# Kernel optimization log

Measured on AMD Instinct MI355X. Metric: run time of the kernel, lower is better.

Reference implementation:

```python
import jax, jax.numpy as jnp
import numpy as np

N = 50000        # num_nodes
E = 800000       # num_edges (avg degree 16)
K = 3            # Chebyshev order
F_IN = 144       # 144 * in_channels
F_OUT = 144      # 144 * out_channels


def setup_inputs() -> dict:
    key = jax.random.key(0)
    k1, k2, k3, k4, k5 = jax.random.split(key, 5)
    x = jax.random.normal(k1, (N, F_IN), dtype=jnp.float32)
    edge_index = jax.random.randint(k2, (2, E), 0, N, dtype=jnp.int32)
    edge_weight = jax.random.uniform(k3, (E,), dtype=jnp.float32)
    weight = jax.random.normal(k4, (K, F_IN, F_OUT), dtype=jnp.float32) * 0.02
    bias = jax.random.normal(k5, (F_OUT,), dtype=jnp.float32) * 0.02
    return {"x": x, "edge_index": edge_index, "edge_weight": edge_weight,
            "weight": weight, "bias": bias}


def reference(x, edge_index, edge_weight, weight, bias):
    row, col = edge_index[0], edge_index[1]
    # remove_self_loops: mask out edges with row == col (fixed-shape equivalent)
    mask = (row != col).astype(x.dtype)
    w = edge_weight * mask
    # degree over remaining edges, deg^-0.5 with inf -> 0
    deg = jax.ops.segment_sum(mask, row, num_segments=N)
    dinv = jnp.where(deg > 0, deg ** -0.5, jnp.zeros_like(deg))
    lap = -dinv[row] * w * dinv[col]  # [E]

    def spmm(v):  # out[i] = sum_{e: row_e = i} lap_e * v[col_e]
        return jax.ops.segment_sum(lap[:, None] * v[col], row, num_segments=N)

    Tx0 = x
    out = Tx0 @ weight[0]
    Tx1 = spmm(Tx0)
    out = out + Tx1 @ weight[1]
    for k in range(2, weight.shape[0]):
        Tx2 = 2.0 * spmm(Tx1) - Tx0
        out = out + Tx2 @ weight[k]
        Tx0, Tx1 = Tx1, Tx2
    return out + bias
```

## Files before the change

### kernel.cpp

```cpp
#include <hip/hip_runtime.h>
#include <hip/hip_bf16.h>

#define NN 50000
#define EE 800000
#define FF 144
#define NBLK 196
#define CVTBLK 1758
#define HISTBLK 3125

typedef __hip_bfloat16 bf16;
typedef __attribute__((ext_vector_type(8))) short short8;
typedef __attribute__((ext_vector_type(4))) float floatx4;
typedef __attribute__((ext_vector_type(2))) float float2v;

__device__ inline float blo(unsigned x) { return __uint_as_float(x << 16); }
__device__ inline float bhi(unsigned x) { return __uint_as_float(x & 0xffff0000u); }

__device__ inline void dec4fma(float* a, float l, unsigned d) {
    float2v p0 = __builtin_amdgcn_cvt_pk_f32_fp8((int)d, false);
    float2v p1 = __builtin_amdgcn_cvt_pk_f32_fp8((int)d, true);
    a[0] = fmaf(l, p0.x, a[0]);
    a[1] = fmaf(l, p0.y, a[1]);
    a[2] = fmaf(l, p1.x, a[2]);
    a[3] = fmaf(l, p1.y, a[3]);
}
__device__ inline void fma16q(float* a, float l, uint4 u) {
    dec4fma(a + 0, l, u.x);
    dec4fma(a + 4, l, u.y);
    dec4fma(a + 8, l, u.z);
    dec4fma(a + 12, l, u.w);
}
__device__ inline unsigned enc4(float a, float b, float c, float d) {
    int w = __builtin_amdgcn_cvt_pk_fp8_f32(a, b, 0, false);
    w = __builtin_amdgcn_cvt_pk_fp8_f32(c, d, w, true);
    return (unsigned)w;
}


__global__ void detect_k(const int* __restrict__ ei, int* __restrict__ flag) {
    __shared__ int nz;
    if (threadIdx.x == 0) nz = 0;
    __syncthreads();
    if (ei[2 * threadIdx.x + 1] != 0) atomicAdd(&nz, 1);
    __syncthreads();
    if (threadIdx.x == 0) *flag = (nz == 0) ? 1 : 0;
}

__device__ inline void load_edge(const int* ei, int e, int flag, int& r, int& c) {
    if (flag) { r = ei[2 * e]; c = ei[2 * EE + 2 * e]; }
    else      { r = ei[e];     c = ei[EE + e]; }
}


__global__ void cvthist_k(const float* __restrict__ x, bf16* __restrict__ xb,
                          unsigned char* __restrict__ xq,
                          const int* __restrict__ ei, int* __restrict__ cnt,
                          unsigned char* __restrict__ rank,
                          const int* __restrict__ flagp) {
    int b = blockIdx.x;
    if (b < CVTBLK) {
        int t = b * 256 + threadIdx.x;
        if (t >= NN * FF / 16) return;
        const float4* xp = (const float4*)x + t * 4;
        float4 v0 = xp[0], v1 = xp[1], v2 = xp[2], v3 = xp[3];
        float f[16] = {v0.x, v0.y, v0.z, v0.w, v1.x, v1.y, v1.z, v1.w,
                       v2.x, v2.y, v2.z, v2.w, v3.x, v3.y, v3.z, v3.w};
        unsigned short hs[16];
        #pragma unroll
        for (int j = 0; j < 16; ++j) {
            bf16 bb = (bf16)f[j];
            hs[j] = *(unsigned short*)&bb;
        }
        uint4* xbq = (uint4*)xb + t * 2;
        xbq[0] = ((uint4*)hs)[0];
        xbq[1] = ((uint4*)hs)[1];
        uint4 q;
        q.x = enc4(f[0], f[1], f[2], f[3]);
        q.y = enc4(f[4], f[5], f[6], f[7]);
        q.z = enc4(f[8], f[9], f[10], f[11]);
        q.w = enc4(f[12], f[13], f[14], f[15]);
        ((uint4*)xq)[t] = q;
    } else {
        int flag = *flagp;
        int e = (b - CVTBLK) * 256 + threadIdx.x;
        if (e >= EE) return;
        int r, c; load_edge(ei, e, flag, r, c);
        if (r != c) rank[e] = (unsigned char)atomicAdd(&cnt[r], 1);
    }
}


__global__ void cvtw_k(const float* __restrict__ wt, short* __restrict__ wtb) {
    int t = blockIdx.x * 256 + threadIdx.x;
    if (t >= 3 * FF * 168) return;
    int ph = t / (FF * 168);
    int rem = t - ph * FF * 168;
    int o = rem / 168;
    int i = rem - o * 168;
    short v = 0;
    if (i < FF) {
        bf16 b = (bf16)wt[ph * FF * FF + i * FF + o];
        v = *(const short*)&b;
    }
    wtb[t] = v;
}


__global__ void scan1_k(const int* __restrict__ cnt, int* __restrict__ rowptr,
                        int* __restrict__ bsum, float* __restrict__ dinv) {
    __shared__ int wsum[4], woff[4];
    int b = blockIdx.x, tid = threadIdx.x;
    int wv = tid >> 6, ln = tid & 63;
    int i = b * 256 + tid;
    int v = (i < NN) ? cnt[i] : 0;
    if (i < NN) dinv[i] = v > 0 ? rsqrtf((float)v) : 0.f;
    int x = v;
    #pragma unroll
    for (int off = 1; off < 64; off <<= 1) {
        int t = __shfl_up(x, off, 64);
        if (ln >= off) x += t;
    }
    if (ln == 63) wsum[wv] = x;
    __syncthreads();
    if (tid == 0) {
        int s = 0;
        #pragma unroll
        for (int j = 0; j < 4; ++j) { woff[j] = s; s += wsum[j]; }
        bsum[b] = s;
    }
    __syncthreads();
    if (i < NN) rowptr[i] = woff[wv] + (x - v);
}

__global__ void scan2_k(int* __restrict__ bsum, int* __restrict__ rowptr) {
    __shared__ int wsum[4], woff[4];
    int tid = threadIdx.x;
    int wv = tid >> 6, ln = tid & 63;
    int v = (tid < NBLK) ? bsum[tid] : 0;
    int x = v;
    #pragma unroll
    for (int off = 1; off < 64; off <<= 1) {
        int t = __shfl_up(x, off, 64);
        if (ln >= off) x += t;
    }
    if (ln == 63) wsum[wv] = x;
    __syncthreads();
    if (tid == 0) {
        int s = 0;
        #pragma unroll
        for (int j = 0; j < 4; ++j) { woff[j] = s; s += wsum[j]; }
        rowptr[NN] = s;
    }
    __syncthreads();
    if (tid < NBLK) bsum[tid] = woff[wv] + (x - v);
}

__global__ void scan3_k(int* __restrict__ rowptr, const int* __restrict__ bsum) {
    int b = blockIdx.x;
    int i = b * 256 + threadIdx.x;
    if (i < NN) rowptr[i] += bsum[b];
}


__global__ void scatter_k(const int* __restrict__ ei, const float* __restrict__ w,
                          const float* __restrict__ dinv, const int* __restrict__ rowptr,
                          const unsigned char* __restrict__ rank,
                          unsigned* __restrict__ pairs, const int* __restrict__ flagp) {
    int flag = *flagp;
    int e = blockIdx.x * 256 + threadIdx.x;
    if (e >= EE) return;
    int r, c; load_edge(ei, e, flag, r, c);
    if (r == c) return;
    int pos = rowptr[r] + (int)rank[e];
    float lap = -dinv[r] * dinv[c] * w[e];
    bf16 lb = (bf16)lap;
    pairs[pos] = (unsigned)c | ((unsigned)*(unsigned short*)&lb << 16);
}


template <int MODE>
__global__ void spmm_k(const unsigned char* __restrict__ vq, const bf16* __restrict__ x0,
                       const int* __restrict__ rowptr, const unsigned* __restrict__ pairs,
                       bf16* __restrict__ y, unsigned char* __restrict__ yq) {
    int t = blockIdx.x * 256 + threadIdx.x;
    if (t >= NN * 9) return;
    int i = t / 9;
    int fo = (t - i * 9) * 16;
    const unsigned char* vp = vq + fo;

    float a[16];
    #pragma unroll
    for (int j = 0; j < 16; ++j) a[j] = 0.f;

    int s = rowptr[i], e = rowptr[i + 1];
    int p = s;
    for (; p + 1 < e; p += 2) {
        unsigned pr0 = pairs[p], pr1 = pairs[p + 1];
        uint4 u0 = *(const uint4*)(vp + (pr0 & 0xffffu) * FF);
        uint4 u1 = *(const uint4*)(vp + (pr1 & 0xffffu) * FF);
        fma16q(a, bhi(pr0), u0);
        fma16q(a, bhi(pr1), u1);
    }
    if (p < e) {
        unsigned pr = pairs[p];
        uint4 u = *(const uint4*)(vp + (pr & 0xffffu) * FF);
        fma16q(a, bhi(pr), u);
    }

    if (MODE == 1) {
        const uint4* xp = (const uint4*)((const unsigned short*)x0 + i * FF + fo);
        uint4 u0 = xp[0], u1 = xp[1];
        a[0]  = 2.f * a[0]  - blo(u0.x);  a[1]  = 2.f * a[1]  - bhi(u0.x);
        a[2]  = 2.f * a[2]  - blo(u0.y);  a[3]  = 2.f * a[3]  - bhi(u0.y);
        a[4]  = 2.f * a[4]  - blo(u0.z);  a[5]  = 2.f * a[5]  - bhi(u0.z);
        a[6]  = 2.f * a[6]  - blo(u0.w);  a[7]  = 2.f * a[7]  - bhi(u0.w);
        a[8]  = 2.f * a[8]  - blo(u1.x);  a[9]  = 2.f * a[9]  - bhi(u1.x);
        a[10] = 2.f * a[10] - blo(u1.y);  a[11] = 2.f * a[11] - bhi(u1.y);
        a[12] = 2.f * a[12] - blo(u1.z);  a[13] = 2.f * a[13] - bhi(u1.z);
        a[14] = 2.f * a[14] - blo(u1.w);  a[15] = 2.f * a[15] - bhi(u1.w);
    }

    unsigned short hs[16];
    #pragma unroll
    for (int j = 0; j < 16; ++j) {
        bf16 b = (bf16)a[j];
        hs[j] = *(unsigned short*)&b;
    }
    uint4* yp = (uint4*)((unsigned short*)y + i * FF + fo);
    yp[0] = ((uint4*)hs)[0];
    yp[1] = ((uint4*)hs)[1];

    if (MODE == 0) {
        uint4 q;
        q.x = enc4(a[0], a[1], a[2], a[3]);
        q.y = enc4(a[4], a[5], a[6], a[7]);
        q.z = enc4(a[8], a[9], a[10], a[11]);
        q.w = enc4(a[12], a[13], a[14], a[15]);
        *(uint4*)(yq + i * FF + fo) = q;
    }
}


__global__ __launch_bounds__(1024)
void gemm_fused(const bf16* __restrict__ A0, const bf16* __restrict__ A1,
                const bf16* __restrict__ A2, const short* __restrict__ wtb,
                const float* __restrict__ bias, float* __restrict__ out) {
    __shared__ __align__(16) short Wt[3 * 144 * 168];
    int tid = threadIdx.x;

    {
        const uint4* Wg = (const uint4*)wtb;
        uint4* Wl = (uint4*)Wt;
        #pragma unroll
        for (int q = 0; q < 9; ++q) {
            int idx = q * 1024 + tid;
            if (idx < 9072) Wl[idx] = Wg[idx];
        }
    }
    __syncthreads();

    int wv = tid >> 6, ln = tid & 63;
    int m16 = ln & 15, quad = ln >> 4;
    int tile = wv * 256 + blockIdx.x;
    if (tile * 16 >= NN) return;
    int rowBase = tile * 16;
    int row = rowBase + m16;

    const bf16* const srcs[3] = {A0, A1, A2};
    const short8 zero8 = {0, 0, 0, 0, 0, 0, 0, 0};

    floatx4 acc[9];
    #pragma unroll
    for (int q = 0; q < 9; ++q) acc[q] = (floatx4){0.f, 0.f, 0.f, 0.f};

    #pragma unroll
    for (int ph = 0; ph < 3; ++ph) {
        const bf16* A = srcs[ph];
        short8 a[5];
        #pragma unroll
        for (int kt = 0; kt < 5; ++kt) {
            int k0 = kt * 32 + quad * 8;
            if (k0 < FF)
                a[kt] = *(const short8*)((const short*)A + row * FF + k0);
            else
                a[kt] = zero8;
        }

        const short* Wp = Wt + ph * 144 * 168;
        #pragma unroll
        for (int nt = 0; nt < 9; ++nt) {
            #pragma unroll
            for (int kt = 0; kt < 5; ++kt) {
                short8 b = *(const short8*)&Wp[(nt * 16 + m16) * 168 + kt * 32 + quad * 8];
                acc[nt] = __builtin_amdgcn_mfma_f32_16x16x32_bf16(a[kt], b, acc[nt], 0, 0, 0);
            }
        }
    }

    int rowc = rowBase + quad * 4;
    #pragma unroll
    for (int nt = 0; nt < 9; ++nt) {
        int col = nt * 16 + m16;
        float bs = bias[col];
        #pragma unroll
        for (int r = 0; r < 4; ++r) {
            int rr = rowc + r;
            out[rr * FF + col] = acc[nt][r] + bs;
        }
    }
}


extern "C" void kernel_launch(void* const* d_in, const int* in_sizes, int n_in,
                              void* d_out, int out_size, void* d_ws, size_t ws_size,
                              hipStream_t stream) {
    int ix = -1, iei = -1, iew = -1, iwt = -1, ib = -1;
    for (int i = 0; i < n_in; ++i) {
        switch (in_sizes[i]) {
            case NN * FF:      if (ix  < 0) ix  = i; break;
            case 2 * EE:       if (iei < 0) iei = i; break;
            case EE:           if (iew < 0) iew = i; break;
            case 3 * FF * FF:  if (iwt < 0) iwt = i; break;
            case FF:           if (ib  < 0) ib  = i; break;
        }
    }
    if (ix < 0 || iei < 0 || iew < 0 || iwt < 0 || ib < 0) {
        ix = 0; iei = 1; iew = 2; iwt = 3; ib = 4;
    }
    const float* x    = (const float*)d_in[ix];
    const int*   ei   = (const int*)d_in[iei];
    const float* ew   = (const float*)d_in[iew];
    const float* wt   = (const float*)d_in[iwt];
    const float* bias = (const float*)d_in[ib];
    float* out = (float*)d_out;

    char* p = (char*)d_ws;
    int*      cnt    = (int*)(p + 0);
    int*      rowptr = (int*)(p + 400000);
    float*    dinv   = (float*)(p + 600016);
    unsigned* pairs  = (unsigned*)(p + 800016);
    unsigned char* rank = (unsigned char*)(p + 4000016);
    bf16*     tx1    = (bf16*)(p + 7200016);
    bf16*     tx2    = (bf16*)(p + 21600016);
    short*    wtb    = (short*)(p + 36000016);
    int*      bsum   = (int*)(p + 36200000);
    unsigned char* xq   = (unsigned char*)(p + 36300000);
    unsigned char* tx1q = (unsigned char*)(p + 43600000);
    bf16*     xb     = (bf16*)(p + 64800016);
    int*      eflag  = (int*)(p + 79200016);

    if (ws_size < 79200032) return;

    hipMemsetAsync(d_ws, 0, 200000, stream);

    int spGrid   = (NN * 9 + 255) / 256;
    int wGrid    = (3 * FF * 168 + 255) / 256;

    detect_k<<<1, 256, 0, stream>>>(ei, eflag);
    cvthist_k<<<CVTBLK + HISTBLK, 256, 0, stream>>>(x, xb, xq, ei, cnt, rank, eflag);
    cvtw_k<<<wGrid, 256, 0, stream>>>(wt, wtb);
    scan1_k<<<NBLK, 256, 0, stream>>>(cnt, rowptr, bsum, dinv);
    scan2_k<<<1, 256, 0, stream>>>(bsum, rowptr);
    scan3_k<<<NBLK, 256, 0, stream>>>(rowptr, bsum);
    scatter_k<<<(EE + 255) / 256, 256, 0, stream>>>(ei, ew, dinv, rowptr, rank, pairs, eflag);

    spmm_k<0><<<spGrid, 256, 0, stream>>>(xq, xb, rowptr, pairs, tx1, tx1q);
    spmm_k<1><<<spGrid, 256, 0, stream>>>(tx1q, xb, rowptr, pairs, tx2, (unsigned char*)0);
    gemm_fused<<<256, 1024, 0, stream>>>(xb, tx1, tx2, wtb, bias, out);
}
```

Baseline: 218.5 us.

## Replace atomic-rank CSR build with two-level bucket sort of edges

Builds the CSR structure with a two-pass bucket sort instead of per-row global atomics. Edges are packed into 64-bit items and histogrammed per chunk into 128-row buckets in shared memory. After a prefix scan they are scattered into coarse buckets, then each bucket is finely sorted with shared-memory atomics to produce rowptr, dinv and the packed pairs. The weight conversion is also fused into the first kernel, the memset is removed, and one scan launch is dropped. In exchange the edge data takes extra passes through 64-bit intermediate buffers, and the order of edges within a row becomes nondeterministic.

```diff
diff --git a/kernel.cpp b/kernel.cpp
--- a/kernel.cpp
+++ b/kernel.cpp
@@ -4,9 +4,14 @@
 #define NN 50000
 #define EE 800000
 #define FF 144
-#define NBLK 196
 #define CVTBLK 1758
-#define HISTBLK 3125
+#define ECHK 2048
+#define NBE 391
+#define NBKT_REAL 391
+#define NBUCKET 392
+#define WGRID 284
+#define HM (NBUCKET * NBE)
+#define SCANBLK 599
 
 typedef __hip_bfloat16 bf16;
 typedef __attribute__((ext_vector_type(8))) short short8;
@@ -52,14 +57,17 @@
 }
 
 
-__global__ void cvthist_k(const float* __restrict__ x, bf16* __restrict__ xb,
-                          unsigned char* __restrict__ xq,
-                          const int* __restrict__ ei, int* __restrict__ cnt,
-                          unsigned char* __restrict__ rank,
-                          const int* __restrict__ flagp) {
+__global__ void fusedA_k(const float* __restrict__ x, bf16* __restrict__ xb,
+                         unsigned char* __restrict__ xq,
+                         const int* __restrict__ ei, const float* __restrict__ ew,
+                         unsigned long long* __restrict__ items, int* __restrict__ hist,
+                         const float* __restrict__ wt, short* __restrict__ wtb,
+                         const int* __restrict__ flagp) {
+    __shared__ int lh[NBUCKET];
     int b = blockIdx.x;
+    int tid = threadIdx.x;
     if (b < CVTBLK) {
-        int t = b * 256 + threadIdx.x;
+        int t = b * 256 + tid;
         if (t >= NN * FF / 16) return;
         const float4* xp = (const float4*)x + t * 4;
         float4 v0 = xp[0], v1 = xp[1], v2 = xp[2], v3 = xp[3];
@@ -80,101 +88,176 @@
         q.z = enc4(f[8], f[9], f[10], f[11]);
         q.w = enc4(f[12], f[13], f[14], f[15]);
         ((uint4*)xq)[t] = q;
+    } else if (b < CVTBLK + NBE) {
+        int bb = b - CVTBLK;
+        for (int j = tid; j < NBUCKET; j += 256) lh[j] = 0;
+        __syncthreads();
+        int flag = *flagp;
+        int eb = bb * ECHK;
+        #pragma unroll
+        for (int k = 0; k < ECHK / 256; ++k) {
+            int e = eb + k * 256 + tid;
+            if (e < EE) {
+                int r, c; load_edge(ei, e, flag, r, c);
+                unsigned key = (r == c) ? 0xFFFFu : (unsigned)r;
+                float w = ew[e];
+                items[e] = ((unsigned long long)((key << 16) | (unsigned)c) << 32)
+                           | (unsigned long long)__float_as_uint(w);
+                atomicAdd(&lh[min(key >> 7, (unsigned)NBKT_REAL)], 1);
+            }
+        }
+        __syncthreads();
+        for (int j = tid; j < NBUCKET; j += 256) hist[j * NBE + bb] = lh[j];
     } else {
-        int flag = *flagp;
-        int e = (b - CVTBLK) * 256 + threadIdx.x;
-        if (e >= EE) return;
-        int r, c; load_edge(ei, e, flag, r, c);
-        if (r != c) rank[e] = (unsigned char)atomicAdd(&cnt[r], 1);
-    }
-}
-
-
-__global__ void cvtw_k(const float* __restrict__ wt, short* __restrict__ wtb) {
-    int t = blockIdx.x * 256 + threadIdx.x;
-    if (t >= 3 * FF * 168) return;
-    int ph = t / (FF * 168);
-    int rem = t - ph * FF * 168;
-    int o = rem / 168;
-    int i = rem - o * 168;
-    short v = 0;
-    if (i < FF) {
-        bf16 b = (bf16)wt[ph * FF * FF + i * FF + o];
-        v = *(const short*)&b;
-    }
-    wtb[t] = v;
-}
-
-
-__global__ void scan1_k(const int* __restrict__ cnt, int* __restrict__ rowptr,
-                        int* __restrict__ bsum, float* __restrict__ dinv) {
+        int t = (b - CVTBLK - NBE) * 256 + tid;
+        if (t >= 3 * FF * 168) return;
+        int ph = t / (FF * 168);
+        int rem = t - ph * FF * 168;
+        int o = rem / 168;
+        int i = rem - o * 168;
+        short v = 0;
+        if (i < FF) {
+            bf16 bv = (bf16)wt[ph * FF * FF + i * FF + o];
+            v = *(const short*)&bv;
+        }
+        wtb[t] = v;
+    }
+}
+
+
+__global__ void scanA1_k(int* __restrict__ hist, int* __restrict__ bsumA) {
     __shared__ int wsum[4], woff[4];
     int b = blockIdx.x, tid = threadIdx.x;
     int wv = tid >> 6, ln = tid & 63;
     int i = b * 256 + tid;
-    int v = (i < NN) ? cnt[i] : 0;
-    if (i < NN) dinv[i] = v > 0 ? rsqrtf((float)v) : 0.f;
-    int x = v;
+    int v = (i < HM) ? hist[i] : 0;
+    int xs = v;
     #pragma unroll
     for (int off = 1; off < 64; off <<= 1) {
-        int t = __shfl_up(x, off, 64);
-        if (ln >= off) x += t;
-    }
-    if (ln == 63) wsum[wv] = x;
+        int t = __shfl_up(xs, off, 64);
+        if (ln >= off) xs += t;
+    }
+    if (ln == 63) wsum[wv] = xs;
     __syncthreads();
     if (tid == 0) {
         int s = 0;
         #pragma unroll
         for (int j = 0; j < 4; ++j) { woff[j] = s; s += wsum[j]; }
-        bsum[b] = s;
-    }
-    __syncthreads();
-    if (i < NN) rowptr[i] = woff[wv] + (x - v);
-}
-
-__global__ void scan2_k(int* __restrict__ bsum, int* __restrict__ rowptr) {
-    __shared__ int wsum[4], woff[4];
-    int tid = threadIdx.x;
-    int wv = tid >> 6, ln = tid & 63;
-    int v = (tid < NBLK) ? bsum[tid] : 0;
-    int x = v;
+        bsumA[b] = s;
+    }
+    __syncthreads();
+    if (i < HM) hist[i] = woff[wv] + (xs - v);
+}
+
+__global__ __launch_bounds__(1024) void scanA2_k(int* __restrict__ bsumA) {
+    __shared__ int wsum[16], woff[16];
+    int tid = threadIdx.x, wv = tid >> 6, ln = tid & 63;
+    int v = (tid < SCANBLK) ? bsumA[tid] : 0;
+    int xs = v;
     #pragma unroll
     for (int off = 1; off < 64; off <<= 1) {
-        int t = __shfl_up(x, off, 64);
-        if (ln >= off) x += t;
-    }
-    if (ln == 63) wsum[wv] = x;
+        int t = __shfl_up(xs, off, 64);
+        if (ln >= off) xs += t;
+    }
+    if (ln == 63) wsum[wv] = xs;
     __syncthreads();
     if (tid == 0) {
         int s = 0;
         #pragma unroll
-        for (int j = 0; j < 4; ++j) { woff[j] = s; s += wsum[j]; }
-        rowptr[NN] = s;
-    }
-    __syncthreads();
-    if (tid < NBLK) bsum[tid] = woff[wv] + (x - v);
-}
-
-__global__ void scan3_k(int* __restrict__ rowptr, const int* __restrict__ bsum) {
-    int b = blockIdx.x;
-    int i = b * 256 + threadIdx.x;
-    if (i < NN) rowptr[i] += bsum[b];
-}
-
-
-__global__ void scatter_k(const int* __restrict__ ei, const float* __restrict__ w,
-                          const float* __restrict__ dinv, const int* __restrict__ rowptr,
-                          const unsigned char* __restrict__ rank,
-                          unsigned* __restrict__ pairs, const int* __restrict__ flagp) {
-    int flag = *flagp;
-    int e = blockIdx.x * 256 + threadIdx.x;
-    if (e >= EE) return;
-    int r, c; load_edge(ei, e, flag, r, c);
-    if (r == c) return;
-    int pos = rowptr[r] + (int)rank[e];
-    float lap = -dinv[r] * dinv[c] * w[e];
-    bf16 lb = (bf16)lap;
-    pairs[pos] = (unsigned)c | ((unsigned)*(unsigned short*)&lb << 16);
+        for (int j = 0; j < 16; ++j) { woff[j] = s; s += wsum[j]; }
+    }
+    __syncthreads();
+    if (tid < SCANBLK) bsumA[tid] = woff[wv] + (xs - v);
+}
+
+__device__ inline int hbase(const int* hist, const int* bsumA, int f) {
+    return hist[f] + bsumA[f >> 8];
+}
+
+
+__global__ void pscat_k(const unsigned long long* __restrict__ items,
+                        const int* __restrict__ hist, const int* __restrict__ bsumA,
+                        unsigned long long* __restrict__ sorted) {
+    __shared__ int lbase[NBUCKET];
+    int b = blockIdx.x, tid = threadIdx.x;
+    for (int j = tid; j < NBUCKET; j += 256) {
+        int f = j * NBE + b;
+        lbase[j] = hbase(hist, bsumA, f);
+    }
+    __syncthreads();
+    int eb = b * ECHK;
+    #pragma unroll
+    for (int k = 0; k < ECHK / 256; ++k) {
+        int e = eb + k * 256 + tid;
+        if (e < EE) {
+            unsigned long long it = items[e];
+            unsigned key = (unsigned)(it >> 48);
+            int bk = (int)min(key >> 7, (unsigned)NBKT_REAL);
+            int slot = atomicAdd(&lbase[bk], 1);
+            sorted[slot] = it;
+        }
+    }
+}
+
+
+__global__ void fine1_k(const unsigned long long* __restrict__ sorted,
+                        const int* __restrict__ hist, const int* __restrict__ bsumA,
+                        int* __restrict__ rowptr, float* __restrict__ dinv) {
+    __shared__ int lh[128];
+    __shared__ int wtot;
+    int b = blockIdx.x, tid = threadIdx.x;
+    if (tid < 128) lh[tid] = 0;
+    int s = hbase(hist, bsumA, b * NBE);
+    int e = hbase(hist, bsumA, (b + 1) * NBE);
+    __syncthreads();
+    for (int p = s + tid; p < e; p += 256)
+        atomicAdd(&lh[(int)(unsigned)(sorted[p] >> 48) - b * 128], 1);
+    __syncthreads();
+    int ln = tid & 63;
+    int v = (tid < 128) ? lh[tid] : 0;
+    int xs = v;
+    #pragma unroll
+    for (int off = 1; off < 64; off <<= 1) {
+        int t = __shfl_up(xs, off, 64);
+        if (ln >= off) xs += t;
+    }
+    if (tid == 63) wtot = xs;
+    __syncthreads();
+    int excl = xs - v + ((tid >= 64 && tid < 128) ? wtot : 0);
+    int gr = b * 128 + tid;
+    if (tid < 128 && gr < NN) {
+        rowptr[gr] = s + excl;
+        dinv[gr] = v > 0 ? rsqrtf((float)v) : 0.f;
+    }
+    if (b == NBKT_REAL - 1 && tid == 0) rowptr[NN] = e;
+}
+
+
+__global__ void fine2_k(const unsigned long long* __restrict__ sorted,
+                        const int* __restrict__ hist, const int* __restrict__ bsumA,
+                        const int* __restrict__ rowptr, const float* __restrict__ dinv,
+                        unsigned* __restrict__ pairs) {
+    __shared__ int lrp[128];
+    __shared__ float ldv[128];
+    int b = blockIdx.x, tid = threadIdx.x;
+    int gr = b * 128 + tid;
+    if (tid < 128) {
+        lrp[tid] = (gr < NN) ? rowptr[gr] : 0;
+        ldv[tid] = (gr < NN) ? dinv[gr] : 0.f;
+    }
+    int s = hbase(hist, bsumA, b * NBE);
+    int e = hbase(hist, bsumA, (b + 1) * NBE);
+    __syncthreads();
+    for (int p = s + tid; p < e; p += 256) {
+        unsigned long long it = sorted[p];
+        int lr = (int)(unsigned)(it >> 48) - b * 128;
+        unsigned c = (unsigned)(it >> 32) & 0xFFFFu;
+        float w = __uint_as_float((unsigned)it);
+        float lap = -ldv[lr] * dinv[c] * w;
+        int slot = atomicAdd(&lrp[lr], 1);
+        bf16 lb = (bf16)lap;
+        pairs[slot] = c | ((unsigned)*(unsigned short*)&lb << 16);
+    }
 }
 
 
@@ -335,34 +418,33 @@
     float* out = (float*)d_out;
 
     char* p = (char*)d_ws;
-    int*      cnt    = (int*)(p + 0);
-    int*      rowptr = (int*)(p + 400000);
-    float*    dinv   = (float*)(p + 600016);
-    unsigned* pairs  = (unsigned*)(p + 800016);
-    unsigned char* rank = (unsigned char*)(p + 4000016);
-    bf16*     tx1    = (bf16*)(p + 7200016);
-    bf16*     tx2    = (bf16*)(p + 21600016);
-    short*    wtb    = (short*)(p + 36000016);
-    int*      bsum   = (int*)(p + 36200000);
-    unsigned char* xq   = (unsigned char*)(p + 36300000);
-    unsigned char* tx1q = (unsigned char*)(p + 43600000);
-    bf16*     xb     = (bf16*)(p + 64800016);
-    int*      eflag  = (int*)(p + 79200016);
-
-    if (ws_size < 79200032) return;
-
-    hipMemsetAsync(d_ws, 0, 200000, stream);
-
-    int spGrid   = (NN * 9 + 255) / 256;
-    int wGrid    = (3 * FF * 168 + 255) / 256;
+    unsigned long long* items  = (unsigned long long*)(p + 0);
+    unsigned long long* sorted = (unsigned long long*)(p + 6400000);
+    int*      hist   = (int*)(p + 12800000);
+    int*      bsumA  = (int*)(p + 13500000);
+    int*      rowptr = (int*)(p + 13600000);
+    float*    dinv   = (float*)(p + 13900000);
+    unsigned* pairs  = (unsigned*)(p + 14200000);
+    int*      eflag  = (int*)(p + 17400000);
+    short*    wtb    = (short*)(p + 17500000);
+    bf16*     tx1    = (bf16*)(p + 17700000);
+    bf16*     tx2    = (bf16*)(p + 32100000);
+    unsigned char* xq   = (unsigned char*)(p + 46500000);
+    unsigned char* tx1q = (unsigned char*)(p + 53700000);
+    bf16*     xb     = (bf16*)(p + 60900000);
+
+    if (ws_size < 75300000) return;
+
+    int spGrid = (NN * 9 + 255) / 256;
 
     detect_k<<<1, 256, 0, stream>>>(ei, eflag);
-    cvthist_k<<<CVTBLK + HISTBLK, 256, 0, stream>>>(x, xb, xq, ei, cnt, rank, eflag);
-    cvtw_k<<<wGrid, 256, 0, stream>>>(wt, wtb);
-    scan1_k<<<NBLK, 256, 0, stream>>>(cnt, rowptr, bsum, dinv);
-    scan2_k<<<1, 256, 0, stream>>>(bsum, rowptr);
-    scan3_k<<<NBLK, 256, 0, stream>>>(rowptr, bsum);
-    scatter_k<<<(EE + 255) / 256, 256, 0, stream>>>(ei, ew, dinv, rowptr, rank, pairs, eflag);
+    fusedA_k<<<CVTBLK + NBE + WGRID, 256, 0, stream>>>(x, xb, xq, ei, ew, items, hist,
+                                                       wt, wtb, eflag);
+    scanA1_k<<<SCANBLK, 256, 0, stream>>>(hist, bsumA);
+    scanA2_k<<<1, 1024, 0, stream>>>(bsumA);
+    pscat_k<<<NBE, 256, 0, stream>>>(items, hist, bsumA, sorted);
+    fine1_k<<<NBKT_REAL, 256, 0, stream>>>(sorted, hist, bsumA, rowptr, dinv);
+    fine2_k<<<NBKT_REAL, 256, 0, stream>>>(sorted, hist, bsumA, rowptr, dinv, pairs);
 
     spmm_k<0><<<spGrid, 256, 0, stream>>>(xq, xb, rowptr, pairs, tx1, tx1q);
     spmm_k<1><<<spGrid, 256, 0, stream>>>(tx1q, xb, rowptr, pairs, tx2, (unsigned char*)0);
```

Result: faster. 189.0 us (-13.5%).
